# Kernel optimization log

Measured on AMD Instinct MI355X. Metric: run time of the kernel, lower is better.

## Reference

```python
import jax, jax.numpy as jnp
import numpy as np

# ---------------- Chu-Liu-Edmonds MST decode (faithful numpy port) ----------------

def _find_cycle(parents, length, current_nodes):
    added = [False] * length
    added[0] = True
    cycle = set()
    has_cycle = False
    for i in range(1, length):
        if has_cycle:
            break
        if added[i] or not current_nodes[i]:
            continue
        this_cycle = {i}
        added[i] = True
        has_cycle = True
        next_node = i
        while parents[next_node] not in this_cycle:
            next_node = parents[next_node]
            if added[next_node]:
                has_cycle = False
                break
            added[next_node] = True
            this_cycle.add(next_node)
        if has_cycle:
            original = next_node
            cycle.add(original)
            next_node = parents[original]
            while next_node != original:
                cycle.add(next_node)
                next_node = parents[next_node]
            break
    return has_cycle, list(cycle)


def chu_liu_edmonds(length, score_matrix, current_nodes, final_edges, old_input, old_output, representatives):
    parents = [-1]
    for node1 in range(1, length):
        parents.append(0)
        if current_nodes[node1]:
            max_score = score_matrix[0, node1]
            for node2 in range(1, length):
                if node2 == node1 or not current_nodes[node2]:
                    continue
                new_score = score_matrix[node2, node1]
                if new_score > max_score:
                    max_score = new_score
                    parents[node1] = node2
    has_cycle, cycle = _find_cycle(parents, length, current_nodes)
    if not has_cycle:
        final_edges[0] = -1
        for node in range(1, length):
            if not current_nodes[node]:
                continue
            parent = old_input[parents[node], node]
            child = old_output[parents[node], node]
            final_edges[child] = parent
        return
    cycle_weight = 0.0
    for node in cycle:
        cycle_weight += score_matrix[parents[node], node]
    cycle_representative = cycle[0]
    for node in range(length):
        if not current_nodes[node] or node in cycle:
            continue
        in_edge_weight = float('-inf')
        in_edge = -1
        out_edge_weight = float('-inf')
        out_edge = -1
        for node_in_cycle in cycle:
            if score_matrix[node_in_cycle, node] > in_edge_weight:
                in_edge_weight = score_matrix[node_in_cycle, node]
                in_edge = node_in_cycle
            score = cycle_weight + score_matrix[node, node_in_cycle] - score_matrix[parents[node_in_cycle], node_in_cycle]
            if score > out_edge_weight:
                out_edge_weight = score
                out_edge = node_in_cycle
        score_matrix[cycle_representative, node] = in_edge_weight
        old_input[cycle_representative, node] = old_input[in_edge, node]
        old_output[cycle_representative, node] = old_output[in_edge, node]
        score_matrix[node, cycle_representative] = out_edge_weight
        old_output[node, cycle_representative] = old_output[node, out_edge]
        old_input[node, cycle_representative] = old_input[node, out_edge]
    considered = []
    for i, node_in_cycle in enumerate(cycle):
        considered.append(set())
        if i > 0:
            current_nodes[node_in_cycle] = False
        for node in representatives[node_in_cycle]:
            considered[i].add(node)
            if i > 0:
                representatives[cycle_representative].add(node)
    chu_liu_edmonds(length, score_matrix, current_nodes, final_edges, old_input, old_output, representatives)
    found = False
    key_node = -1
    for i, node in enumerate(cycle):
        for cycle_rep in considered[i]:
            if cycle_rep in final_edges:
                key_node = node
                found = True
                break
        if found:
            break
    previous = parents[key_node]
    while previous != key_node:
        child = old_output[parents[previous], previous]
        parent = old_input[parents[previous], previous]
        final_edges[child] = parent
        previous = parents[previous]


def decode_mst(energy, length):
    # energy: numpy [num_labels, T, T]
    max_length = energy.shape[-1]
    energy = energy[:, :length, :length]
    label_id_matrix = energy.argmax(axis=0)
    score_matrix = np.array(energy.max(axis=0), copy=True)
    old_input = np.zeros([length, length], dtype=np.int32)
    old_output = np.zeros([length, length], dtype=np.int32)
    current_nodes = [True] * length
    representatives = []
    for node1 in range(length):
        score_matrix[node1, node1] = 0.0
        representatives.append({node1})
        for node2 in range(node1 + 1, length):
            old_input[node1, node2] = node1
            old_output[node1, node2] = node2
            old_input[node2, node1] = node2
            old_output[node2, node1] = node1
    final_edges = {}
    chu_liu_edmonds(length, score_matrix, current_nodes, final_edges, old_input, old_output, representatives)
    heads = np.zeros([max_length], np.int32)
    head_type = np.ones([max_length], np.int32)
    for child, parent in final_edges.items():
        heads[child] = parent
        head_type[child] = label_id_matrix[parent, child]
    return heads, head_type


# ---------------- biaffine scoring (jax) ----------------

@jax.jit
def _energy(encoded_text, W_head_arc, b_head_arc, W_dep_arc, b_dep_arc, U_arc,
            W_head_lab, b_head_lab, W_dep_lab, b_dep_lab, U_lab):
    h_arc = jax.nn.elu(encoded_text @ W_head_arc + b_head_arc)   # [B,T,A]
    d_arc = jax.nn.elu(encoded_text @ W_dep_arc + b_dep_arc)     # [B,T,A]
    arc_scores = jnp.einsum('bia,ac,bjc->bij', h_arc, U_arc, d_arc)  # head i -> dep j
    h_lab = jax.nn.elu(encoded_text @ W_head_lab + b_head_lab)   # [B,T,R]
    d_lab = jax.nn.elu(encoded_text @ W_dep_lab + b_dep_lab)     # [B,T,R]
    lab_scores = jnp.einsum('bir,lrs,bjs->blij', h_lab, U_lab, d_lab)  # [B,L,T,T]
    norm_arc = jax.nn.log_softmax(arc_scores, axis=1)   # normalize over heads
    norm_lab = jax.nn.log_softmax(lab_scores, axis=1)   # normalize over labels
    return jnp.exp(norm_arc[:, None, :, :] + norm_lab)  # [B,L,T,T] edge energies


def setup_inputs() -> dict:
    key = jax.random.key(0)
    ks = jax.random.split(key, 8)
    B, T, D, A, R, L = 32, 128, 768, 512, 128, 50
    s = 0.02
    return {
        'encoded_text': jax.random.normal(ks[0], (B, T, D), jnp.float32),
        'W_head_arc': jax.random.normal(ks[1], (D, A), jnp.float32) * s,
        'b_head_arc': jnp.zeros((A,), jnp.float32),
        'W_dep_arc': jax.random.normal(ks[2], (D, A), jnp.float32) * s,
        'b_dep_arc': jnp.zeros((A,), jnp.float32),
        'U_arc': jax.random.normal(ks[3], (A, A), jnp.float32) * s,
        'W_head_lab': jax.random.normal(ks[4], (D, R), jnp.float32) * s,
        'b_head_lab': jnp.zeros((R,), jnp.float32),
        'W_dep_lab': jax.random.normal(ks[5], (D, R), jnp.float32) * s,
        'b_dep_lab': jnp.zeros((R,), jnp.float32),
        'U_lab': jax.random.normal(ks[6], (L, R, R), jnp.float32) * s,
        'mask': jnp.ones((B, T), jnp.bool_),
    }


def reference(encoded_text, W_head_arc, b_head_arc, W_dep_arc, b_dep_arc, U_arc,
              W_head_lab, b_head_lab, W_dep_lab, b_dep_lab, U_lab, mask):
    energy = _energy(encoded_text, W_head_arc, b_head_arc, W_dep_arc, b_dep_arc, U_arc,
                     W_head_lab, b_head_lab, W_dep_lab, b_dep_lab, U_lab)
    lengths = np.asarray(mask.sum(-1))
    energy_np = np.asarray(energy)
    heads, tags = [], []
    # per-example Chu-Liu-Edmonds decode (inherently sequential, as in the original)
    for i in range(energy_np.shape[0]):
        h, t = decode_mst(energy_np[i], int(lengths[i]))
        heads.append(h)
        tags.append(t)
    return energy, jnp.asarray(np.stack(heads)), jnp.asarray(np.stack(tags))
```

## Files before the change

### kernel.cpp

```cpp
#include <hip/hip_runtime.h>
#include <math.h>

#define B_ 32
#define T_ 128
#define D_ 768
#define A_ 512
#define R_ 128
#define L_ 50

__global__ __launch_bounds__(256)
void proj_gemm_k(const float* __restrict__ X,
                 const float* __restrict__ Wha, const float* __restrict__ bha,
                 const float* __restrict__ Wda, const float* __restrict__ bda,
                 const float* __restrict__ Whl, const float* __restrict__ bhl,
                 const float* __restrict__ Wdl, const float* __restrict__ bdl,
                 float* __restrict__ HA, float* __restrict__ DA,
                 float* __restrict__ HL, float* __restrict__ DL)
{
    __shared__ float As[16][68];
    __shared__ float Bs[16][132];
    const int bx = blockIdx.x;
    const float *W, *bias; float* C; int ld, ncol;
    if (bx < 4)      { W = Wha; bias = bha; C = HA; ld = 512; ncol = bx * 128; }
    else if (bx < 8) { W = Wda; bias = bda; C = DA; ld = 512; ncol = (bx - 4) * 128; }
    else if (bx == 8){ W = Whl; bias = bhl; C = HL; ld = 128; ncol = 0; }
    else             { W = Wdl; bias = bdl; C = DL; ld = 128; ncol = 0; }
    const int m0 = blockIdx.y * 64;
    const int tid = threadIdx.x;
    const int tx = tid & 15, ry = tid >> 4;
    float acc[4][8] = {};
    for (int k0 = 0; k0 < 768; k0 += 16) {
        {
            int row = tid >> 2, kb = (tid & 3) * 4;
            float4 a = *(const float4*)&X[(size_t)(m0 + row) * 768 + k0 + kb];
            As[kb + 0][row] = a.x; As[kb + 1][row] = a.y;
            As[kb + 2][row] = a.z; As[kb + 3][row] = a.w;
        }
        {
            int kk = tid >> 4, c0 = (tid & 15) * 4;
            const float* Bp = &W[(size_t)(k0 + kk) * ld + ncol + c0];
            *(float4*)&Bs[kk][c0] = *(const float4*)&Bp[0];
            *(float4*)&Bs[kk][c0 + 64] = *(const float4*)&Bp[64];
        }
        __syncthreads();
#pragma unroll
        for (int kk = 0; kk < 16; ++kk) {
            float4 a4 = *(const float4*)&As[kk][ry * 4];
            float4 b0 = *(const float4*)&Bs[kk][tx * 4];
            float4 b1 = *(const float4*)&Bs[kk][tx * 4 + 64];
            float av[4] = { a4.x, a4.y, a4.z, a4.w };
            float bv[8] = { b0.x, b0.y, b0.z, b0.w, b1.x, b1.y, b1.z, b1.w };
#pragma unroll
            for (int i = 0; i < 4; ++i)
#pragma unroll
                for (int j = 0; j < 8; ++j)
                    acc[i][j] += av[i] * bv[j];
        }
        __syncthreads();
    }
    float bv0[8];
    {
        float4 q0 = *(const float4*)&bias[ncol + tx * 4];
        float4 q1 = *(const float4*)&bias[ncol + tx * 4 + 64];
        bv0[0] = q0.x; bv0[1] = q0.y; bv0[2] = q0.z; bv0[3] = q0.w;
        bv0[4] = q1.x; bv0[5] = q1.y; bv0[6] = q1.z; bv0[7] = q1.w;
    }
#pragma unroll
    for (int i = 0; i < 4; ++i) {
        int m = m0 + ry * 4 + i;
        size_t base = (size_t)m * ld + ncol;
        float o[8];
#pragma unroll
        for (int j = 0; j < 8; ++j) {
            float v = acc[i][j] + bv0[j];
            o[j] = v > 0.0f ? v : expm1f(v);
        }
        float4 s0 = { o[0], o[1], o[2], o[3] };
        float4 s1 = { o[4], o[5], o[6], o[7] };
        *(float4*)&C[base + tx * 4] = s0;
        *(float4*)&C[base + tx * 4 + 64] = s1;
    }
}

__global__ __launch_bounds__(256)
void gemm_k(const float* __restrict__ A, const float* __restrict__ B,
            const float* __restrict__ bias, float* __restrict__ C,
            int K, int lda, int ldb, int ldc,
            long long sA, long long sB, long long sC, long long c_outer, int flags)
{
    __shared__ float As[16][68];
    __shared__ float Bs[16][132];
    A += (size_t)blockIdx.z * sA;
    B += (size_t)blockIdx.z * sB;
    C += (size_t)blockIdx.z * sC;
    const int m0 = blockIdx.y * 64, n0 = blockIdx.x * 128;
    const int tid = threadIdx.x;
    const int tx = tid & 15, ry = tid >> 4;
    float acc[4][8] = {};
    for (int k0 = 0; k0 < K; k0 += 16) {
        {
            int row = tid >> 2, kb = (tid & 3) * 4;
            float4 a = *(const float4*)&A[(size_t)(m0 + row) * lda + k0 + kb];
            As[kb + 0][row] = a.x; As[kb + 1][row] = a.y;
            As[kb + 2][row] = a.z; As[kb + 3][row] = a.w;
        }
        if (!(flags & 4)) {
            int kk = tid >> 4, c0 = (tid & 15) * 4;
            const float* Bp = &B[(size_t)(k0 + kk) * ldb + n0 + c0];
            *(float4*)&Bs[kk][c0] = *(const float4*)&Bp[0];
            *(float4*)&Bs[kk][c0 + 64] = *(const float4*)&Bp[64];
        } else {
            int col = tid >> 1, kb = (tid & 1) * 8;
            const float* Bp = &B[(size_t)(n0 + col) * ldb + k0 + kb];
            float4 b0 = *(const float4*)&Bp[0];
            float4 b1 = *(const float4*)&Bp[4];
            Bs[kb + 0][col] = b0.x; Bs[kb + 1][col] = b0.y;
            Bs[kb + 2][col] = b0.z; Bs[kb + 3][col] = b0.w;
            Bs[kb + 4][col] = b1.x; Bs[kb + 5][col] = b1.y;
            Bs[kb + 6][col] = b1.z; Bs[kb + 7][col] = b1.w;
        }
        __syncthreads();
#pragma unroll
        for (int kk = 0; kk < 16; ++kk) {
            float4 a4 = *(const float4*)&As[kk][ry * 4];
            float4 b0 = *(const float4*)&Bs[kk][tx * 4];
            float4 b1 = *(const float4*)&Bs[kk][tx * 4 + 64];
            float av[4] = { a4.x, a4.y, a4.z, a4.w };
            float bv[8] = { b0.x, b0.y, b0.z, b0.w, b1.x, b1.y, b1.z, b1.w };
#pragma unroll
            for (int i = 0; i < 4; ++i)
#pragma unroll
                for (int j = 0; j < 8; ++j)
                    acc[i][j] += av[i] * bv[j];
        }
        __syncthreads();
    }
    float bv0[8] = {};
    if (flags & 1) {
        float4 q0 = *(const float4*)&bias[n0 + tx * 4];
        float4 q1 = *(const float4*)&bias[n0 + tx * 4 + 64];
        bv0[0] = q0.x; bv0[1] = q0.y; bv0[2] = q0.z; bv0[3] = q0.w;
        bv0[4] = q1.x; bv0[5] = q1.y; bv0[6] = q1.z; bv0[7] = q1.w;
    }
#pragma unroll
    for (int i = 0; i < 4; ++i) {
        int m = m0 + ry * 4 + i;
        size_t base = (size_t)(m >> 7) * c_outer + (size_t)(m & 127) * ldc + n0;
        float o[8];
#pragma unroll
        for (int j = 0; j < 8; ++j) {
            float v = acc[i][j] + bv0[j];
            if (flags & 2) v = v > 0.0f ? v : expm1f(v);
            o[j] = v;
        }
        float4 s0 = { o[0], o[1], o[2], o[3] };
        float4 s1 = { o[4], o[5], o[6], o[7] };
        *(float4*)&C[base + tx * 4] = s0;
        *(float4*)&C[base + tx * 4 + 64] = s1;
    }
}

__global__ __launch_bounds__(256)
void transpose_k(const float* __restrict__ in, float* __restrict__ out)
{
    __shared__ float tile[32][33];
    int b = blockIdx.z;
    int bx = blockIdx.x, by = blockIdx.y;
    int tx = threadIdx.x, ty = threadIdx.y;
    const float* src = in + (size_t)b * T_ * R_;
    float* dst = out + (size_t)b * T_ * R_;
#pragma unroll
    for (int r = 0; r < 4; ++r)
        tile[ty + 8 * r][tx] = src[(size_t)(by * 32 + ty + 8 * r) * 128 + bx * 32 + tx];
    __syncthreads();
#pragma unroll
    for (int r = 0; r < 4; ++r)
        dst[(size_t)(bx * 32 + ty + 8 * r) * 128 + by * 32 + tx] = tile[tx][ty + 8 * r];
}

__global__ __launch_bounds__(128)
void arc_logsoftmax_k(float* __restrict__ arc)
{
    int b = blockIdx.x, j = threadIdx.x;
    float* base = arc + (size_t)b * T_ * T_ + j;
    float m = -INFINITY;
    for (int i = 0; i < T_; ++i) m = fmaxf(m, base[(size_t)i * T_]);
    float s = 0.0f;
    for (int i = 0; i < T_; ++i) s += expf(base[(size_t)i * T_] - m);
    float ls = m + logf(s);
    for (int i = 0; i < T_; ++i) base[(size_t)i * T_] -= ls;
}

__global__ __launch_bounds__(256)
void lab_inplace_k(float* __restrict__ E, const float* __restrict__ dlt)
{
    __shared__ __align__(16) float As[T_ * R_];
    int l = blockIdx.x, b = blockIdx.y;
    float* base = E + ((size_t)b * L_ + l) * T_ * T_;
    int tid = threadIdx.x;
#pragma unroll
    for (int it = 0; it < 16; ++it) {
        int idx = (it * 256 + tid) * 4;
        *(float4*)&As[idx] = *(const float4*)&base[idx];
    }
    __syncthreads();
    int tx = tid & 15, ty = tid >> 4;
    int j0 = tx * 8, i0 = ty * 8;
    const float* dl = dlt + (size_t)b * T_ * R_;
    float acc[8][8] = {};
    for (int s0 = 0; s0 < R_; s0 += 4) {
        float a[8][4], bb[4][8];
#pragma unroll
        for (int ii = 0; ii < 8; ++ii) {
            float4 v = *(const float4*)&As[(i0 + ii) * R_ + s0];
            a[ii][0] = v.x; a[ii][1] = v.y; a[ii][2] = v.z; a[ii][3] = v.w;
        }
#pragma unroll
        for (int ss = 0; ss < 4; ++ss) {
            float4 x = *(const float4*)&dl[(size_t)(s0 + ss) * T_ + j0];
            float4 y = *(const float4*)&dl[(size_t)(s0 + ss) * T_ + j0 + 4];
            bb[ss][0] = x.x; bb[ss][1] = x.y; bb[ss][2] = x.z; bb[ss][3] = x.w;
            bb[ss][4] = y.x; bb[ss][5] = y.y; bb[ss][6] = y.z; bb[ss][7] = y.w;
        }
#pragma unroll
        for (int ii = 0; ii < 8; ++ii)
#pragma unroll
            for (int jj = 0; jj < 8; ++jj)
#pragma unroll
                for (int ss = 0; ss < 4; ++ss)
                    acc[ii][jj] += a[ii][ss] * bb[ss][jj];
    }
#pragma unroll
    for (int ii = 0; ii < 8; ++ii) {
        float4 o0 = { acc[ii][0], acc[ii][1], acc[ii][2], acc[ii][3] };
        float4 o1 = { acc[ii][4], acc[ii][5], acc[ii][6], acc[ii][7] };
        *(float4*)&base[(size_t)(i0 + ii) * T_ + j0] = o0;
        *(float4*)&base[(size_t)(i0 + ii) * T_ + j0 + 4] = o1;
    }
}

__global__ __launch_bounds__(256)
void energy_combine_k(float* __restrict__ E, const float* __restrict__ narc,
                      float* __restrict__ score_g, unsigned char* __restrict__ labmax_g)
{
    int g = blockIdx.x * 256 + threadIdx.x;
    int b = g >> 14;
    int ij = g & 16383;
    float* base = E + (size_t)b * L_ * T_ * T_ + ij;
    float v[L_];
    float m = -INFINITY;
    int am = 0;
#pragma unroll
    for (int l = 0; l < L_; ++l) {
        v[l] = base[(size_t)l * T_ * T_];
        if (v[l] > m) { m = v[l]; am = l; }
    }
    float s = 0.0f;
#pragma unroll
    for (int l = 0; l < L_; ++l) s += expf(v[l] - m);
    float ls = m + logf(s);
    float na = narc[(size_t)b * T_ * T_ + ij];
#pragma unroll
    for (int l = 0; l < L_; ++l) base[(size_t)l * T_ * T_] = expf(na + v[l] - ls);
    int i = ij >> 7, j = ij & 127;
    score_g[(size_t)b * 16384 + ij] = (i == j) ? 0.0f : expf(na + m - ls);
    labmax_g[(size_t)b * 16384 + ij] = (unsigned char)am;
}

__global__ __launch_bounds__(256)
void mst_k(const float* __restrict__ score_g, const unsigned char* __restrict__ labmax_g,
           float* __restrict__ heads, float* __restrict__ tags)
{
    const int b = blockIdx.x, t = threadIdx.x;
    __shared__ float score[128 * 129];
    __shared__ unsigned short oio[128 * 129];
    __shared__ unsigned char pstL[96 * 128];
    __shared__ unsigned char kynL[96 * 128];
    __shared__ int parents[128];
    __shared__ int fe[128];
    __shared__ float pmx[128];
    __shared__ int pp[128];
    __shared__ float cwacc[128];
    __shared__ int cnt[128];
    __shared__ int offarr[128];
    __shared__ float Lsub[128];
    __shared__ unsigned char Lnode[128], Lcid[128];
    __shared__ unsigned char cidarr[128], oncyc[128];

    {
        const float4* src = (const float4*)(score_g + (size_t)b * 16384);
        for (int i = t; i < 4096; i += 256) {
            float4 v = src[i];
            int r = i >> 5, c = (i & 31) * 4;
            float* d = &score[r * 129 + c];
            d[0] = v.x; d[1] = v.y; d[2] = v.z; d[3] = v.w;
        }
    }
    for (int i = t; i < 16384; i += 256) {
        int r = i >> 7, c = i & 127;
        oio[r * 129 + c] = (unsigned short)(r | (c << 8));
    }
    if (t < 128) { fe[t] = -2; oncyc[t] = 0; }
    __syncthreads();
    if (t < 128) score[t * 129 + t] = -INFINITY;
    __syncthreads();
    float mxl = 0.0f; int pl = 0;
    if (t >= 128) {
        int col = t - 128;
        float mx = -INFINITY; int pu = 64;
        if (col != 0) {
            mx = score[64 * 129 + col];
#pragma unroll 16
            for (int n2 = 65; n2 < 128; ++n2) {
                float sc = score[n2 * 129 + col];
                if (sc > mx) { mx = sc; pu = n2; }
            }
        }
        pmx[col] = mx; pp[col] = pu;
    } else if (t != 0) {
        mxl = score[t]; pl = 0;
#pragma unroll 16
        for (int n2 = 1; n2 < 64; ++n2) {
            float sc = score[n2 * 129 + t];
            if (sc > mxl) { mxl = sc; pl = n2; }
        }
    }
    __syncthreads();
    if (t == 0) parents[0] = -1;
    else if (t < 128) parents[t] = (pmx[t] > mxl) ? pp[t] : pl;
    __syncthreads();

    if (t < 64) {
        const int n0 = t, n1 = t + 64;
        int p0 = parents[n0], p1 = parents[n1];
        int c0 = 1, c1 = 1;
        int r0 = n0, r1 = n1;
        int lev = 0, nact = 128, pass = 0;
        for (;;) {
            int rounds = 32 - __clz(nact - 1);
            int a0 = (n0 == 0 || !c0) ? 0 : p0;
            int a1 = (!c1) ? 0 : p1;
            int m0 = n0, m1 = n1;
            for (int s = 0; s < rounds; ++s) {
                int pk0 = (a0 << 7) | m0;
                int pk1 = (a1 << 7) | m1;
                int q00 = __shfl(pk0, a0 & 63, 64);
                int q01 = __shfl(pk1, a0 & 63, 64);
                int q10 = __shfl(pk0, a1 & 63, 64);
                int q11 = __shfl(pk1, a1 & 63, 64);
                int g0 = (a0 & 64) ? q01 : q00;
                int g1 = (a1 & 64) ? q11 : q10;
                a0 = g0 >> 7; int gm0 = g0 & 127; m0 = gm0 < m0 ? gm0 : m0;
                a1 = g1 >> 7; int gm1 = g1 & 127; m1 = gm1 < m1 ? gm1 : m1;
            }
            int pred0 = (n0 >= 1) && c0 && (a0 != 0);
            int pred1 = c1 && (a1 != 0);
            unsigned long long bal0 = __ballot(pred0);
            unsigned long long bal1 = __ballot(pred1);
            if (bal0 == 0ull && bal1 == 0ull) {
                if (n0 == 0) fe[0] = -1;
                else if (c0) { int w = oio[p0 * 129 + n0]; fe[w >> 8] = w & 255; }
                if (c1) { int w = oio[p1 * 129 + n1]; fe[w >> 8] = w & 255; }
                __threadfence_block();
                break;
            }
            unsigned char ep = (unsigned char)(++pass);
            if (pred0) oncyc[a0] = ep;
            if (pred1) oncyc[a1] = ep;
            cnt[n0] = 0; cnt[n1] = 0;
            cwacc[n0] = 0.0f; cwacc[n1] = 0.0f;
            __threadfence_block();
            int onc0 = c0 && (oncyc[n0] == ep);
            int onc1 = c1 && (oncyc[n1] == ep);
            const int cid0 = m0, cid1 = m1;
            cidarr[n0] = onc0 ? (unsigned char)cid0 : 0xFF;
            cidarr[n1] = onc1 ? (unsigned char)cid1 : 0xFF;
            float sub0 = 0.0f, sub1 = 0.0f;
            int rk0 = 0, rk1 = 0;
            if (onc0) { sub0 = score[p0 * 129 + n0]; rk0 = atomicAdd(&cnt[cid0], 1); atomicAdd(&cwacc[cid0], sub0); }
            if (onc1) { sub1 = score[p1 * 129 + n1]; rk1 = atomicAdd(&cnt[cid1], 1); atomicAdd(&cwacc[cid1], sub1); }
            __threadfence_block();
            int x0 = cnt[n0], x1 = cnt[n1];
            int v = (x0 & 0xFFFF) | (x1 << 16);
            for (int off = 1; off < 64; off <<= 1) {
                int u = __shfl(v, t >= off ? t - off : 0, 64);
                v += (t >= off) ? u : 0;
            }
            int tot = __shfl(v, 63, 64);
            int Mtot = (tot & 0xFFFF) + (tot >> 16);
            offarr[n0] = (v & 0xFFFF) - x0;
            offarr[n1] = (tot & 0xFFFF) + ((v >> 16) & 0xFFFF) - x1;
            __threadfence_block();
            if (onc0) { int sl = offarr[cid0] + rk0; Lnode[sl] = (unsigned char)n0; Lcid[sl] = (unsigned char)cid0; Lsub[sl] = sub0; }
            if (onc1) { int sl = offarr[cid1] + rk1; Lnode[sl] = (unsigned char)n1; Lcid[sl] = (unsigned char)cid1; Lsub[sl] = sub1; }
            int rc0 = cidarr[r0], rc1 = cidarr[r1];
            if (lev < 96) {
                pstL[lev * 128 + n0] = (unsigned char)p0;
                pstL[lev * 128 + n1] = (unsigned char)p1;
                kynL[lev * 128 + n0] = (rc0 != 0xFF) ? (unsigned char)r0 : 0xFF;
                kynL[lev * 128 + n1] = (rc1 != 0xFF) ? (unsigned char)r1 : 0xFF;
            }
            if (rc0 != 0xFF) r0 = rc0;
            if (rc1 != 0xFF) r1 = rc1;
            __threadfence_block();
            {
                int lim0 = c0 ? (onc0 ? cid0 : 256) : -1;
                int lim1 = c1 ? (onc1 ? cid1 : 256) : -1;
                float inw0 = -INFINITY, outw0 = -INFINITY;
                float inw1 = -INFINITY, outw1 = -INFINITY;
                int qi0 = 0, qo0 = 0, qi1 = 0, qo1 = 0;
                int cidC = Lcid[0], mC = Lnode[0];
                float sbC = Lsub[0];
                for (int i = 0; i < Mtot; ++i) {
                    int cidN = 0, mN = 0; float sbN = 0.0f;
                    if (i + 1 < Mtot) { cidN = Lcid[i + 1]; mN = Lnode[i + 1]; sbN = Lsub[i + 1]; }
                    if (cidC < lim0) {
                        float si = score[mC * 129 + n0];
                        float so = score[n0 * 129 + mC] - sbC;
                        int wi = oio[mC * 129 + n0];
                        int wo = oio[n0 * 129 + mC];
                        if (si > inw0) { inw0 = si; qi0 = wi; }
                        if (so > outw0) { outw0 = so; qo0 = wo; }
                    }
                    if (cidC < lim1) {
                        float si = score[mC * 129 + n1];
                        float so = score[n1 * 129 + mC] - sbC;
                        int wi = oio[mC * 129 + n1];
                        int wo = oio[n1 * 129 + mC];
                        if (si > inw1) { inw1 = si; qi1 = wi; }
                        if (so > outw1) { outw1 = so; qo1 = wo; }
                    }
                    int segend = (i + 1 == Mtot) || (cidN != cidC);
                    if (segend) {
                        if (cidC < lim0) {
                            float cwc = cwacc[cidC];
                            score[cidC * 129 + n0] = inw0; oio[cidC * 129 + n0] = (unsigned short)qi0;
                            score[n0 * 129 + cidC] = cwc + outw0; oio[n0 * 129 + cidC] = (unsigned short)qo0;
                        }
                        if (cidC < lim1) {
                            float cwc = cwacc[cidC];
                            score[cidC * 129 + n1] = inw1; oio[cidC * 129 + n1] = (unsigned short)qi1;
                            score[n1 * 129 + cidC] = cwc + outw1; oio[n1 * 129 + cidC] = (unsigned short)qo1;
                        }
                        inw0 = -INFINITY; outw0 = -INFINITY;
                        inw1 = -INFINITY; outw1 = -INFINITY;
                    }
                    cidC = cidN; mC = mN; sbC = sbN;
                }
            }
            __threadfence_block();
            int rp0 = onc0 && (n0 == cid0);
            int rp1 = onc1 && (n1 == cid1);
            unsigned long long q0 = __ballot(rp0);
            unsigned long long q1 = __ballot(rp1);
            int ncyc = (int)__popcll(q0) + (int)__popcll(q1);
            if (ncyc >= 2) {
                float inw0 = -INFINITY, outw0 = -INFINITY;
                float inw1 = -INFINITY, outw1 = -INFINITY;
                int qi0 = 0, qo0 = 0, qi1 = 0, qo1 = 0;
                int cidC = Lcid[0], mC = Lnode[0];
                float sbC = Lsub[0];
                for (int i = 0; i < Mtot; ++i) {
                    int cidN = 0, mN = 0; float sbN = 0.0f;
                    if (i + 1 < Mtot) { cidN = Lcid[i + 1]; mN = Lnode[i + 1]; sbN = Lsub[i + 1]; }
                    int e0 = rp0 && (cidC > cid0);
                    int e1 = rp1 && (cidC > cid1);
                    if (e0) {
                        float si = score[mC * 129 + n0];
                        float so = score[n0 * 129 + mC] - sbC;
                        int wi = oio[mC * 129 + n0];
                        int wo = oio[n0 * 129 + mC];
                        if (si > inw0) { inw0 = si; qi0 = wi; }
                        if (so > outw0) { outw0 = so; qo0 = wo; }
                    }
                    if (e1) {
                        float si = score[mC * 129 + n1];
                        float so = score[n1 * 129 + mC] - sbC;
                        int wi = oio[mC * 129 + n1];
                        int wo = oio[n1 * 129 + mC];
                        if (si > inw1) { inw1 = si; qi1 = wi; }
                        if (so > outw1) { outw1 = so; qo1 = wo; }
                    }
                    int segend = (i + 1 == Mtot) || (cidN != cidC);
                    if (segend) {
                        if (e0) {
                            float cwc = cwacc[cidC];
                            score[cidC * 129 + n0] = inw0; oio[cidC * 129 + n0] = (unsigned short)qi0;
                            score[n0 * 129 + cidC] = cwc + outw0; oio[n0 * 129 + cidC] = (unsigned short)qo0;
                        }
                        if (e1) {
                            float cwc = cwacc[cidC];
                            score[cidC * 129 + n1] = inw1; oio[cidC * 129 + n1] = (unsigned short)qi1;
                            score[n1 * 129 + cidC] = cwc + outw1; oio[n1 * 129 + cidC] = (unsigned short)qo1;
                        }
                        inw0 = -INFINITY; outw0 = -INFINITY;
                        inw1 = -INFINITY; outw1 = -INFINITY;
                    }
                    cidC = cidN; mC = mN; sbC = sbN;
                }
                __threadfence_block();
            }
            if (onc0 && n0 != cid0) c0 = 0;
            if (onc1 && n1 != cid1) c1 = 0;
            if (c0 && n0 != 0) { int cp = cidarr[p0]; if (cp != 0xFF) p0 = cp; }
            if (c1)            { int cp = cidarr[p1]; if (cp != 0xFF) p1 = cp; }
            {
                unsigned long long w0 = q0, w1 = q1;
                while (w0 | w1) {
                    int repA, repB = -1;
                    if (w0) { repA = (int)__ffsll((long long)w0) - 1; w0 &= w0 - 1; }
                    else    { repA = 64 + (int)__ffsll((long long)w1) - 1; w1 &= w1 - 1; }
                    if (w0) { repB = (int)__ffsll((long long)w0) - 1; w0 &= w0 - 1; }
                    else if (w1) { repB = 64 + (int)__ffsll((long long)w1) - 1; w1 &= w1 - 1; }
                    float aA = c0 ? score[n0 * 129 + repA] : -INFINITY;
                    float bA = c1 ? score[n1 * 129 + repA] : -INFINITY;
                    float aB = -INFINITY, bB = -INFINITY;
                    if (repB >= 0) {
                        aB = c0 ? score[n0 * 129 + repB] : -INFINITY;
                        bB = c1 ? score[n1 * 129 + repB] : -INFINITY;
                    }
                    float vA; int iA;
                    if (bA > aA) { vA = bA; iA = n1; } else { vA = aA; iA = n0; }
                    float vB; int iB;
                    if (bB > aB) { vB = bB; iB = n1; } else { vB = aB; iB = n0; }
#pragma unroll
                    for (int off = 32; off >= 1; off >>= 1) {
                        float oA = __shfl_xor(vA, off, 64);
                        int jA = __shfl_xor(iA, off, 64);
                        float oB = __shfl_xor(vB, off, 64);
                        int jB = __shfl_xor(iB, off, 64);
                        if (oA > vA || (oA == vA && jA < iA)) { vA = oA; iA = jA; }
                        if (oB > vB || (oB == vB && jB < iB)) { vB = oB; iB = jB; }
                    }
                    if (n0 == repA) p0 = iA;
                    if (n1 == repA) p1 = iA;
                    if (repB >= 0) {
                        if (n0 == repB) p0 = iB;
                        if (n1 == repB) p1 = iB;
                    }
                }
            }
            nact -= (Mtot - ncyc);
            ++lev;
        }
        int ltop = lev < 96 ? lev : 96;
        for (int l2 = ltop - 1; l2 >= 0; --l2) {
            int ky0 = kynL[l2 * 128 + n0], ky1 = kynL[l2 * 128 + n1];
            int cand0 = (ky0 != 0xFF) && (fe[n0] != -2);
            int cand1 = (ky1 != 0xFF) && (fe[n1] != -2);
            if (cand0) {
                int key = ky0;
                int prev = pstL[l2 * 128 + key];
                int guard = 0;
                while (prev != key && guard++ < 130) {
                    int pp2 = pstL[l2 * 128 + prev];
                    int w = oio[pp2 * 129 + prev];
                    fe[w >> 8] = w & 255;
                    prev = pp2;
                }
            }
            if (cand1) {
                int key = ky1;
                int prev = pstL[l2 * 128 + key];
                int guard = 0;
                while (prev != key && guard++ < 130) {
                    int pp2 = pstL[l2 * 128 + prev];
                    int w = oio[pp2 * 129 + prev];
                    fe[w >> 8] = w & 255;
                    prev = pp2;
                }
            }
            __threadfence_block();
        }
    }
    __syncthreads();

    if (t < 128) {
        int f = fe[t];
        float h, ht;
        if (f != -2) {
            h = (float)f;
            int prow = (f < 0) ? 127 : f;
            ht = (float)(int)labmax_g[(size_t)b * 16384 + prow * 128 + t];
        } else { h = 0.0f; ht = 1.0f; }
        heads[b * 128 + t] = h;
        tags[b * 128 + t] = ht;
    }
}

extern "C" void kernel_launch(void* const* d_in, const int* in_sizes, int n_in,
                              void* d_out, int out_size, void* d_ws, size_t ws_size,
                              hipStream_t stream)
{
    const float* X   = (const float*)d_in[0];
    const float* Wha = (const float*)d_in[1];
    const float* bha = (const float*)d_in[2];
    const float* Wda = (const float*)d_in[3];
    const float* bda = (const float*)d_in[4];
    const float* Ua  = (const float*)d_in[5];
    const float* Whl = (const float*)d_in[6];
    const float* bhl = (const float*)d_in[7];
    const float* Wdl = (const float*)d_in[8];
    const float* bdl = (const float*)d_in[9];
    const float* Ul  = (const float*)d_in[10];

    char* ws = (char*)d_ws;
    float* HA    = (float*)(ws + (size_t)0);
    float* DA    = (float*)(ws + ((size_t)8 << 20));
    float* TA    = (float*)(ws + ((size_t)16 << 20));
    float* HL    = (float*)(ws + ((size_t)24 << 20));
    float* DL    = (float*)(ws + ((size_t)26 << 20));
    float* DLt   = (float*)(ws + ((size_t)28 << 20));
    float* ARC   = (float*)(ws + ((size_t)30 << 20));
    float* SCORE = (float*)(ws + ((size_t)32 << 20));
    unsigned char* LABMAX = (unsigned char*)(ws + ((size_t)34 << 20));

    float* E     = (float*)d_out;
    float* heads = E + (size_t)B_ * L_ * T_ * T_;
    float* tags  = heads + (size_t)B_ * T_;

    dim3 thr(256);
    proj_gemm_k<<<dim3(10, 64), thr, 0, stream>>>(X, Wha, bha, Wda, bda, Whl, bhl, Wdl, bdl,
                                                  HA, DA, HL, DL);
    gemm_k<<<dim3(4, 64, 1), thr, 0, stream>>>(HA, Ua, nullptr, TA, 512, 512, 512, 512, 0, 0, 0, (long long)128 * 512, 0);
    transpose_k<<<dim3(4, 4, 32), dim3(32, 8), 0, stream>>>(DL, DLt);
    gemm_k<<<dim3(1, 2, 32), thr, 0, stream>>>(TA, DA, nullptr, ARC, 512, 512, 512, 128, 65536, 65536, 16384, 0, 4);
    arc_logsoftmax_k<<<32, 128, 0, stream>>>(ARC);
    gemm_k<<<dim3(1, 64, 50), thr, 0, stream>>>(HL, Ul, nullptr, E, 128, 128, 128, 128, 0, 16384, 16384, (long long)50 * 16384, 0);
    lab_inplace_k<<<dim3(50, 32), thr, 0, stream>>>(E, DLt);
    energy_combine_k<<<2048, 256, 0, stream>>>(E, ARC, SCORE, LABMAX);
    mst_k<<<32, 256, 0, stream>>>(SCORE, LABMAX, heads, tags);
}
```

Baseline: 894.7 us.

## Fuse label bilinear GEMMs into one kernel keeping intermediate in LDS

Replaces the two-stage label energy computation (a global GEMM writing HL·U_l into E, then an in-place second GEMM with DL^T) with a single kernel per (label, batch) block. It computes the first product into shared memory and then multiplies by the transposed dependent projection before writing E once. This removes one full write and read of the large B×L×T×T intermediate and one kernel launch. In exchange each block uses about 76 KB of LDS, which lowers occupancy, and it recomputes the first GEMM tile-staged with extra syncs.

```diff
diff --git a/kernel.cpp b/kernel.cpp
--- a/kernel.cpp
+++ b/kernel.cpp
@@ -192,50 +192,96 @@
 }
 
 __global__ __launch_bounds__(256)
-void lab_inplace_k(float* __restrict__ E, const float* __restrict__ dlt)
-{
-    __shared__ __align__(16) float As[T_ * R_];
-    int l = blockIdx.x, b = blockIdx.y;
-    float* base = E + ((size_t)b * L_ + l) * T_ * T_;
-    int tid = threadIdx.x;
-#pragma unroll
-    for (int it = 0; it < 16; ++it) {
-        int idx = (it * 256 + tid) * 4;
-        *(float4*)&As[idx] = *(const float4*)&base[idx];
-    }
-    __syncthreads();
-    int tx = tid & 15, ty = tid >> 4;
-    int j0 = tx * 8, i0 = ty * 8;
-    const float* dl = dlt + (size_t)b * T_ * R_;
+void tl_lab_k(const float* __restrict__ HL, const float* __restrict__ Ul,
+              const float* __restrict__ dlt, float* __restrict__ E)
+{
+    __shared__ float T[128 * 132];
+    __shared__ float stg[16][132];
+    const int l = blockIdx.x, b = blockIdx.y;
+    const int t = threadIdx.x;
+    const int tx = t & 15, ty = t >> 4;
+    const int j0 = tx * 8, i0 = ty * 8;
+    const float* Apan = HL + (size_t)b * 128 * 128;
+    const float* Bpan = Ul + (size_t)l * 16384;
+    const float* Dpan = dlt + (size_t)b * 16384;
     float acc[8][8] = {};
-    for (int s0 = 0; s0 < R_; s0 += 4) {
-        float a[8][4], bb[4][8];
-#pragma unroll
-        for (int ii = 0; ii < 8; ++ii) {
-            float4 v = *(const float4*)&As[(i0 + ii) * R_ + s0];
-            a[ii][0] = v.x; a[ii][1] = v.y; a[ii][2] = v.z; a[ii][3] = v.w;
-        }
-#pragma unroll
-        for (int ss = 0; ss < 4; ++ss) {
-            float4 x = *(const float4*)&dl[(size_t)(s0 + ss) * T_ + j0];
-            float4 y = *(const float4*)&dl[(size_t)(s0 + ss) * T_ + j0 + 4];
-            bb[ss][0] = x.x; bb[ss][1] = x.y; bb[ss][2] = x.z; bb[ss][3] = x.w;
-            bb[ss][4] = y.x; bb[ss][5] = y.y; bb[ss][6] = y.z; bb[ss][7] = y.w;
-        }
-#pragma unroll
-        for (int ii = 0; ii < 8; ++ii)
-#pragma unroll
-            for (int jj = 0; jj < 8; ++jj)
-#pragma unroll
-                for (int ss = 0; ss < 4; ++ss)
-                    acc[ii][jj] += a[ii][ss] * bb[ss][jj];
+    for (int k0 = 0; k0 < 128; k0 += 8) {
+        {
+            int row = t & 127, kb = (t >> 7) * 4;
+            float4 a = *(const float4*)&Apan[row * 128 + k0 + kb];
+            stg[kb + 0][row] = a.x; stg[kb + 1][row] = a.y;
+            stg[kb + 2][row] = a.z; stg[kb + 3][row] = a.w;
+            int kk = t >> 5, c4 = (t & 31) * 4;
+            *(float4*)&stg[8 + kk][c4] = *(const float4*)&Bpan[(size_t)(k0 + kk) * 128 + c4];
+        }
+        __syncthreads();
+#pragma unroll
+        for (int kk = 0; kk < 8; ++kk) {
+            float4 a0 = *(const float4*)&stg[kk][i0];
+            float4 a1 = *(const float4*)&stg[kk][i0 + 4];
+            float4 b0 = *(const float4*)&stg[8 + kk][j0];
+            float4 b1 = *(const float4*)&stg[8 + kk][j0 + 4];
+            float av[8] = { a0.x, a0.y, a0.z, a0.w, a1.x, a1.y, a1.z, a1.w };
+            float bv[8] = { b0.x, b0.y, b0.z, b0.w, b1.x, b1.y, b1.z, b1.w };
+#pragma unroll
+            for (int i = 0; i < 8; ++i)
+#pragma unroll
+                for (int j = 0; j < 8; ++j)
+                    acc[i][j] += av[i] * bv[j];
+        }
+        __syncthreads();
     }
 #pragma unroll
     for (int ii = 0; ii < 8; ++ii) {
         float4 o0 = { acc[ii][0], acc[ii][1], acc[ii][2], acc[ii][3] };
         float4 o1 = { acc[ii][4], acc[ii][5], acc[ii][6], acc[ii][7] };
-        *(float4*)&base[(size_t)(i0 + ii) * T_ + j0] = o0;
-        *(float4*)&base[(size_t)(i0 + ii) * T_ + j0 + 4] = o1;
+        *(float4*)&T[(i0 + ii) * 132 + j0] = o0;
+        *(float4*)&T[(i0 + ii) * 132 + j0 + 4] = o1;
+#pragma unroll
+        for (int j = 0; j < 8; ++j) acc[ii][j] = 0.0f;
+    }
+    __syncthreads();
+    for (int s0 = 0; s0 < 128; s0 += 16) {
+        {
+            int kk = t >> 4, c8 = (t & 15) * 8;
+            *(float4*)&stg[kk][c8] = *(const float4*)&Dpan[(size_t)(s0 + kk) * 128 + c8];
+            *(float4*)&stg[kk][c8 + 4] = *(const float4*)&Dpan[(size_t)(s0 + kk) * 128 + c8 + 4];
+        }
+        __syncthreads();
+#pragma unroll
+        for (int sh = 0; sh < 4; ++sh) {
+            int sb = sh * 4;
+            float a[8][4];
+#pragma unroll
+            for (int ii = 0; ii < 8; ++ii) {
+                float4 v = *(const float4*)&T[(i0 + ii) * 132 + s0 + sb];
+                a[ii][0] = v.x; a[ii][1] = v.y; a[ii][2] = v.z; a[ii][3] = v.w;
+            }
+            float bb[4][8];
+#pragma unroll
+            for (int ss = 0; ss < 4; ++ss) {
+                float4 x = *(const float4*)&stg[sb + ss][j0];
+                float4 y = *(const float4*)&stg[sb + ss][j0 + 4];
+                bb[ss][0] = x.x; bb[ss][1] = x.y; bb[ss][2] = x.z; bb[ss][3] = x.w;
+                bb[ss][4] = y.x; bb[ss][5] = y.y; bb[ss][6] = y.z; bb[ss][7] = y.w;
+            }
+#pragma unroll
+            for (int ii = 0; ii < 8; ++ii)
+#pragma unroll
+                for (int jj = 0; jj < 8; ++jj)
+#pragma unroll
+                    for (int ss = 0; ss < 4; ++ss)
+                        acc[ii][jj] += a[ii][ss] * bb[ss][jj];
+        }
+        __syncthreads();
+    }
+    float* base = E + ((size_t)b * L_ + l) * 16384;
+#pragma unroll
+    for (int ii = 0; ii < 8; ++ii) {
+        float4 o0 = { acc[ii][0], acc[ii][1], acc[ii][2], acc[ii][3] };
+        float4 o1 = { acc[ii][4], acc[ii][5], acc[ii][6], acc[ii][7] };
+        *(float4*)&base[(size_t)(i0 + ii) * 128 + j0] = o0;
+        *(float4*)&base[(size_t)(i0 + ii) * 128 + j0 + 4] = o1;
     }
 }
 
@@ -626,8 +672,7 @@
     transpose_k<<<dim3(4, 4, 32), dim3(32, 8), 0, stream>>>(DL, DLt);
     gemm_k<<<dim3(1, 2, 32), thr, 0, stream>>>(TA, DA, nullptr, ARC, 512, 512, 512, 128, 65536, 65536, 16384, 0, 4);
     arc_logsoftmax_k<<<32, 128, 0, stream>>>(ARC);
-    gemm_k<<<dim3(1, 64, 50), thr, 0, stream>>>(HL, Ul, nullptr, E, 128, 128, 128, 128, 0, 16384, 16384, (long long)50 * 16384, 0);
-    lab_inplace_k<<<dim3(50, 32), thr, 0, stream>>>(E, DLt);
+    tl_lab_k<<<dim3(50, 32), thr, 0, stream>>>(HL, Ul, DLt, E);
     energy_combine_k<<<2048, 256, 0, stream>>>(E, ARC, SCORE, LABMAX);
     mst_k<<<32, 256, 0, stream>>>(SCORE, LABMAX, heads, tags);
 }
```

Measured after the change: 957.3 us. +7.0%, slower.

## Fuse label bilinear GEMMs into one kernel keeping intermediate in shared memory

Applied to the files above, without the earlier changes.

Replaces the separate HL·U_lab GEMM, which wrote its intermediate into E, and the in-place second GEMM with DLt with a single kernel. That kernel computes a 64-row slice of the first product into shared memory and immediately multiplies it by DLt. This removes one full write and read of the large B×L×T×T intermediate buffer and one launch. In exchange it uses more shared memory per block, which may lower occupancy, and each block recomputes only its own slice.

```diff
diff --git a/kernel.cpp b/kernel.cpp
--- a/kernel.cpp
+++ b/kernel.cpp
@@ -192,50 +192,88 @@
 }
 
 __global__ __launch_bounds__(256)
-void lab_inplace_k(float* __restrict__ E, const float* __restrict__ dlt)
-{
-    __shared__ __align__(16) float As[T_ * R_];
-    int l = blockIdx.x, b = blockIdx.y;
-    float* base = E + ((size_t)b * L_ + l) * T_ * T_;
-    int tid = threadIdx.x;
-#pragma unroll
-    for (int it = 0; it < 16; ++it) {
-        int idx = (it * 256 + tid) * 4;
-        *(float4*)&As[idx] = *(const float4*)&base[idx];
+void tl_lab_k(const float* __restrict__ HL, const float* __restrict__ Ul,
+              const float* __restrict__ dlt, float* __restrict__ E)
+{
+    __shared__ float Ts[128 * 68];
+    __shared__ float As[16][68];
+    __shared__ float Bs[16][132];
+    const int l = blockIdx.x, b = blockIdx.y;
+    const int m0 = blockIdx.z * 64;
+    const int tid = threadIdx.x;
+    const int tx = tid & 15, ry = tid >> 4;
+    const float* Apan = HL + (size_t)b * 16384 + (size_t)m0 * 128;
+    const float* Bpan = Ul + (size_t)l * 16384;
+    const float* Dpan = dlt + (size_t)b * 16384;
+    float acc[4][8] = {};
+    for (int k0 = 0; k0 < 128; k0 += 16) {
+        {
+            int row = tid >> 2, kb = (tid & 3) * 4;
+            float4 a = *(const float4*)&Apan[(size_t)row * 128 + k0 + kb];
+            As[kb + 0][row] = a.x; As[kb + 1][row] = a.y;
+            As[kb + 2][row] = a.z; As[kb + 3][row] = a.w;
+        }
+        {
+            int kk = tid >> 4, c0 = (tid & 15) * 4;
+            const float* Bp = &Bpan[(size_t)(k0 + kk) * 128 + c0];
+            *(float4*)&Bs[kk][c0] = *(const float4*)&Bp[0];
+            *(float4*)&Bs[kk][c0 + 64] = *(const float4*)&Bp[64];
+        }
+        __syncthreads();
+#pragma unroll
+        for (int kk = 0; kk < 16; ++kk) {
+            float4 a4 = *(const float4*)&As[kk][ry * 4];
+            float4 b0 = *(const float4*)&Bs[kk][tx * 4];
+            float4 b1 = *(const float4*)&Bs[kk][tx * 4 + 64];
+            float av[4] = { a4.x, a4.y, a4.z, a4.w };
+            float bv[8] = { b0.x, b0.y, b0.z, b0.w, b1.x, b1.y, b1.z, b1.w };
+#pragma unroll
+            for (int i = 0; i < 4; ++i)
+#pragma unroll
+                for (int j = 0; j < 8; ++j)
+                    acc[i][j] += av[i] * bv[j];
+        }
+        __syncthreads();
+    }
+#pragma unroll
+    for (int j = 0; j < 8; ++j) {
+        int col = (j < 4) ? (tx * 4 + j) : (64 + tx * 4 + j - 4);
+        float4 w = { acc[0][j], acc[1][j], acc[2][j], acc[3][j] };
+        *(float4*)&Ts[col * 68 + ry * 4] = w;
+#pragma unroll
+        for (int i = 0; i < 4; ++i) acc[i][j] = 0.0f;
     }
     __syncthreads();
-    int tx = tid & 15, ty = tid >> 4;
-    int j0 = tx * 8, i0 = ty * 8;
-    const float* dl = dlt + (size_t)b * T_ * R_;
-    float acc[8][8] = {};
-    for (int s0 = 0; s0 < R_; s0 += 4) {
-        float a[8][4], bb[4][8];
-#pragma unroll
-        for (int ii = 0; ii < 8; ++ii) {
-            float4 v = *(const float4*)&As[(i0 + ii) * R_ + s0];
-            a[ii][0] = v.x; a[ii][1] = v.y; a[ii][2] = v.z; a[ii][3] = v.w;
-        }
-#pragma unroll
-        for (int ss = 0; ss < 4; ++ss) {
-            float4 x = *(const float4*)&dl[(size_t)(s0 + ss) * T_ + j0];
-            float4 y = *(const float4*)&dl[(size_t)(s0 + ss) * T_ + j0 + 4];
-            bb[ss][0] = x.x; bb[ss][1] = x.y; bb[ss][2] = x.z; bb[ss][3] = x.w;
-            bb[ss][4] = y.x; bb[ss][5] = y.y; bb[ss][6] = y.z; bb[ss][7] = y.w;
-        }
-#pragma unroll
-        for (int ii = 0; ii < 8; ++ii)
-#pragma unroll
-            for (int jj = 0; jj < 8; ++jj)
-#pragma unroll
-                for (int ss = 0; ss < 4; ++ss)
-                    acc[ii][jj] += a[ii][ss] * bb[ss][jj];
-    }
-#pragma unroll
-    for (int ii = 0; ii < 8; ++ii) {
-        float4 o0 = { acc[ii][0], acc[ii][1], acc[ii][2], acc[ii][3] };
-        float4 o1 = { acc[ii][4], acc[ii][5], acc[ii][6], acc[ii][7] };
-        *(float4*)&base[(size_t)(i0 + ii) * T_ + j0] = o0;
-        *(float4*)&base[(size_t)(i0 + ii) * T_ + j0 + 4] = o1;
+    for (int k0 = 0; k0 < 128; k0 += 16) {
+        {
+            int kk = tid >> 4, c0 = (tid & 15) * 4;
+            const float* Bp = &Dpan[(size_t)(k0 + kk) * 128 + c0];
+            *(float4*)&Bs[kk][c0] = *(const float4*)&Bp[0];
+            *(float4*)&Bs[kk][c0 + 64] = *(const float4*)&Bp[64];
+        }
+        __syncthreads();
+#pragma unroll
+        for (int kk = 0; kk < 16; ++kk) {
+            float4 a4 = *(const float4*)&Ts[(k0 + kk) * 68 + ry * 4];
+            float4 b0 = *(const float4*)&Bs[kk][tx * 4];
+            float4 b1 = *(const float4*)&Bs[kk][tx * 4 + 64];
+            float av[4] = { a4.x, a4.y, a4.z, a4.w };
+            float bv[8] = { b0.x, b0.y, b0.z, b0.w, b1.x, b1.y, b1.z, b1.w };
+#pragma unroll
+            for (int i = 0; i < 4; ++i)
+#pragma unroll
+                for (int j = 0; j < 8; ++j)
+                    acc[i][j] += av[i] * bv[j];
+        }
+        __syncthreads();
+    }
+    float* base = E + ((size_t)b * L_ + l) * 16384 + (size_t)m0 * 128;
+#pragma unroll
+    for (int i = 0; i < 4; ++i) {
+        float4 s0 = { acc[i][0], acc[i][1], acc[i][2], acc[i][3] };
+        float4 s1 = { acc[i][4], acc[i][5], acc[i][6], acc[i][7] };
+        *(float4*)&base[(size_t)(ry * 4 + i) * 128 + tx * 4] = s0;
+        *(float4*)&base[(size_t)(ry * 4 + i) * 128 + tx * 4 + 64] = s1;
     }
 }
 
@@ -626,8 +664,7 @@
     transpose_k<<<dim3(4, 4, 32), dim3(32, 8), 0, stream>>>(DL, DLt);
     gemm_k<<<dim3(1, 2, 32), thr, 0, stream>>>(TA, DA, nullptr, ARC, 512, 512, 512, 128, 65536, 65536, 16384, 0, 4);
     arc_logsoftmax_k<<<32, 128, 0, stream>>>(ARC);
-    gemm_k<<<dim3(1, 64, 50), thr, 0, stream>>>(HL, Ul, nullptr, E, 128, 128, 128, 128, 0, 16384, 16384, (long long)50 * 16384, 0);
-    lab_inplace_k<<<dim3(50, 32), thr, 0, stream>>>(E, DLt);
+    tl_lab_k<<<dim3(50, 32, 2), thr, 0, stream>>>(HL, Ul, DLt, E);
     energy_combine_k<<<2048, 256, 0, stream>>>(E, ARC, SCORE, LABMAX);
     mst_k<<<32, 256, 0, stream>>>(SCORE, LABMAX, heads, tags);
 }
```

Result: no change. 882.6 us (median of 2 runs) (-1.4%).
